# Kernel optimization log

Hardware: AMD Instinct MI355X
Metric: run time of the kernel (lower is better)

## Reference

```python
import jax, jax.numpy as jnp
import numpy as np
import math

B, S, D, H = 2, 2048, 1024, 16
DK = D // H

def setup_inputs() -> dict:
    key = jax.random.key(0)
    ks = jax.random.split(key, 12)
    sc = 1.0 / math.sqrt(D)
    q = jax.random.normal(ks[0], (B, S, D), jnp.float32)
    k = jax.random.normal(ks[1], (B, S, D), jnp.float32)
    v = jax.random.normal(ks[2], (B, S, D), jnp.float32)
    # causal mask, broadcast over batch and heads; 0 -> masked (filled with -100)
    mask = jnp.tril(jnp.ones((S, S), jnp.int32))[None, None, :, :]
    w_q = jax.random.normal(ks[3], (D, D), jnp.float32) * sc
    b_q = jnp.zeros((D,), jnp.float32)
    w_k = jax.random.normal(ks[4], (D, D), jnp.float32) * sc
    b_k = jnp.zeros((D,), jnp.float32)
    w_v = jax.random.normal(ks[5], (D, D), jnp.float32) * sc
    b_v = jnp.zeros((D,), jnp.float32)
    w_0 = jax.random.normal(ks[6], (D, D), jnp.float32) * sc
    b_0 = jnp.zeros((D,), jnp.float32)
    return {"q": q, "k": k, "v": v, "mask": mask,
            "w_q": w_q, "b_q": b_q, "w_k": w_k, "b_k": b_k,
            "w_v": w_v, "b_v": b_v, "w_0": w_0, "b_0": b_0}

def reference(q, k, v, mask, w_q, b_q, w_k, b_k, w_v, b_v, w_0, b_0):
    # projections (nn.Linear: x @ W^T + b)
    query = q @ w_q.T + b_q              # [B,S,D]
    key_ = k @ w_k.T + b_k
    value = v @ w_v.T + b_v
    # split heads -> [B,H,S,DK]
    def split(x):
        return x.reshape(B, S, H, DK).transpose(0, 2, 1, 3)
    Q, K, V = split(query), split(key_), split(value)
    scores = jnp.einsum('bhqd,bhkd->bhqk', Q, K) / math.sqrt(DK)
    scores = jnp.where(mask == 0, jnp.float32(-100.0), scores)
    attn = jax.nn.softmax(scores, axis=-1)   # dropout p=0.0 -> identity
    out = jnp.einsum('bhqk,bhkd->bhqd', attn, V)  # [B,H,S,DK]
    out = out.transpose(0, 2, 1, 3).reshape(B, S, D)
    return out @ w_0.T + b_0
```

## Files before the change

kernel.cpp:

```cpp
#include <hip/hip_runtime.h>
#include <hip/hip_bf16.h>


namespace {

typedef unsigned short u16;
typedef unsigned int u32;
typedef short bf16x8 __attribute__((ext_vector_type(8)));
typedef float f32x4 __attribute__((ext_vector_type(4)));
typedef int i32x4 __attribute__((ext_vector_type(4)));

constexpr int Bz = 2, Sq = 2048, Dm = 1024, Hh = 16, Dk = 64;
constexpr int Mr = Bz * Sq;

__device__ __forceinline__ u16 bfh(float f) {
  return __bfloat16_as_ushort(__float2bfloat16(f));
}
__device__ __forceinline__ float bfup(u16 u) {
  return __uint_as_float((u32)u << 16);
}

__device__ __forceinline__ void global_load_lds16(const u16* g, u16* lds) {
  __builtin_amdgcn_global_load_lds(
      (const __attribute__((address_space(1))) void*)g,
      (__attribute__((address_space(3))) void*)lds, 16, 0, 0);
}

struct ConvArgs {
  const float* s[7]; u16* hi[7]; u16* lo[7]; int n[7];
};

__global__ __launch_bounds__(256)
void convert_hilo(ConvArgs a) {
  const int z = blockIdx.y;
  const int n = a.n[z];
  const int i = (blockIdx.x * 256 + threadIdx.x) * 4;
  if (i >= n) return;
  const float4 v = *(const float4*)(a.s[z] + i);
  ushort4 h, l;
  h.x = bfh(v.x); l.x = bfh(v.x - bfup(h.x));
  h.y = bfh(v.y); l.y = bfh(v.y - bfup(h.y));
  h.z = bfh(v.z); l.z = bfh(v.z - bfup(h.z));
  h.w = bfh(v.w); l.w = bfh(v.w - bfup(h.w));
  *(ushort4*)(a.hi[z] + i) = h;
  *(ushort4*)(a.lo[z] + i) = l;
}

template<int OUT>
__device__ __forceinline__ void gemm_split_body(
    const u16* __restrict__ Ahi, const u16* __restrict__ Alo,
    const u16* __restrict__ Bhi, const u16* __restrict__ Blo,
    const float* __restrict__ bias, float scale,
    u16* __restrict__ Yh, u16* __restrict__ Yl, float* __restrict__ Yf)
{
  constexpr int K = 1024;
  __shared__ u16 lAh[4096], lAl[4096], lBh[4096], lBl[4096];

  const int t = threadIdx.x;
  const int w = t >> 6, l = t & 63;
  const int m0 = blockIdx.x * 128, n0 = blockIdx.y * 128;
  const int wm = (w >> 1) * 64, wn = (w & 1) * 64;
  const int kg = l >> 4, lr = l & 15;

  f32x4 acc[4][4] = {};

  for (int k0 = 0; k0 < K; k0 += 32) {
#pragma unroll
    for (int is = 0; is < 2; ++is) {
      const int s = is * 256 + w * 64 + l;
      const int row = s & 127, g = s >> 7;
      const size_t aoff = (size_t)(m0 + row) * K + k0 + g * 8;
      const size_t boff = (size_t)(n0 + row) * K + k0 + g * 8;
      const int ldso = (is * 256 + w * 64) * 8;
      global_load_lds16(Ahi + aoff, &lAh[ldso]);
      global_load_lds16(Alo + aoff, &lAl[ldso]);
      global_load_lds16(Bhi + boff, &lBh[ldso]);
      global_load_lds16(Blo + boff, &lBl[ldso]);
    }
    __syncthreads();

    bf16x8 ah[4], al[4], bh[4], bl[4];
#pragma unroll
    for (int f = 0; f < 4; ++f) {
      const int ai = kg * 1024 + (wm + f * 16 + lr) * 8;
      const int bi = kg * 1024 + (wn + f * 16 + lr) * 8;
      ah[f] = *(const bf16x8*)&lAh[ai];
      al[f] = *(const bf16x8*)&lAl[ai];
      bh[f] = *(const bf16x8*)&lBh[bi];
      bl[f] = *(const bf16x8*)&lBl[bi];
    }
#pragma unroll
    for (int mf = 0; mf < 4; ++mf)
#pragma unroll
      for (int nf = 0; nf < 4; ++nf) {
        acc[mf][nf] = __builtin_amdgcn_mfma_f32_16x16x32_bf16(ah[mf], bh[nf], acc[mf][nf], 0, 0, 0);
        acc[mf][nf] = __builtin_amdgcn_mfma_f32_16x16x32_bf16(ah[mf], bl[nf], acc[mf][nf], 0, 0, 0);
        acc[mf][nf] = __builtin_amdgcn_mfma_f32_16x16x32_bf16(al[mf], bh[nf], acc[mf][nf], 0, 0, 0);
      }
    __syncthreads();
  }

#pragma unroll
  for (int mf = 0; mf < 4; ++mf)
#pragma unroll
    for (int nf = 0; nf < 4; ++nf) {
      const int n = n0 + wn + nf * 16 + lr;
      const float bv = bias[n];
      const int mbase = m0 + wm + mf * 16 + kg * 4;
      if (OUT == 2) {
#pragma unroll
        for (int r = 0; r < 4; ++r)
          Yf[(size_t)(mbase + r) * Dm + n] = (acc[mf][nf][r] + bv) * scale;
      } else {
        u16 hi[4], lo[4];
#pragma unroll
        for (int r = 0; r < 4; ++r) {
          const float val = (acc[mf][nf][r] + bv) * scale;
          hi[r] = bfh(val);
          lo[r] = bfh(val - bfup(hi[r]));
        }
        const int bb = mbase >> 11;
        const int hh = n >> 6, dkk = n & (Dk - 1);
        if (OUT == 0) {
          const size_t base = ((size_t)(bb * Hh + hh) * Sq + (mbase & (Sq - 1))) * Dk + dkk;
#pragma unroll
          for (int r = 0; r < 4; ++r) {
            Yh[base + (size_t)r * Dk] = hi[r];
            Yl[base + (size_t)r * Dk] = lo[r];
          }
        } else {
          const size_t base = ((size_t)(bb * Hh + hh) * Dk + dkk) * Sq + (mbase & (Sq - 1));
          ushort4 H, L;
          H.x = hi[0]; H.y = hi[1]; H.z = hi[2]; H.w = hi[3];
          L.x = lo[0]; L.y = lo[1]; L.z = lo[2]; L.w = lo[3];
          *(ushort4*)(Yh + base) = H;
          *(ushort4*)(Yl + base) = L;
        }
      }
    }
}

__global__ __launch_bounds__(256, 2)
void gemm_qkv_split(const u16* xqh, const u16* xql, const u16* xkh, const u16* xkl,
                    const u16* xvh, const u16* xvl,
                    const u16* wqh, const u16* wql, const u16* wkh, const u16* wkl,
                    const u16* wvh, const u16* wvl,
                    const float* bq, const float* bk, const float* bv,
                    u16* Qhi, u16* Qlo, u16* Khi, u16* Klo, u16* Vthi, u16* Vtlo)
{
  const int z = blockIdx.z;
  if (z == 0)
    gemm_split_body<0>(xqh, xql, wqh, wql, bq, 0.125f, Qhi, Qlo, nullptr);
  else if (z == 1)
    gemm_split_body<0>(xkh, xkl, wkh, wkl, bk, 1.0f, Khi, Klo, nullptr);
  else
    gemm_split_body<1>(xvh, xvl, wvh, wvl, bv, 1.0f, Vthi, Vtlo, nullptr);
}

__global__ __launch_bounds__(256, 2)
void gemm_out_split(const u16* Ah, const u16* Al, const u16* Bh, const u16* Bl,
                    const float* bias, float* Y)
{
  gemm_split_body<2>(Ah, Al, Bh, Bl, bias, 1.0f, nullptr, nullptr, Y);
}

__global__ __launch_bounds__(256, 3)
void attn_mfma(const u16* __restrict__ Qhi, const u16* __restrict__ Qlo,
               const u16* __restrict__ Khi, const u16* __restrict__ Klo,
               const u16* __restrict__ Vthi, const u16* __restrict__ Vtlo,
               u16* __restrict__ ctxh, u16* __restrict__ ctxl)
{
  __shared__ u16 stg[2 * 8192];

  const int qt = blockIdx.x, h = blockIdx.y, b = blockIdx.z;
  const int w = threadIdx.x >> 6, l = threadIdx.x & 63;
  const int lr = l & 15, g = l >> 4;
  const int q0 = qt * 64;
  const int myq = q0 + w + 4 * lr;
  const size_t hoff  = (size_t)(b * Hh + h) * Sq * Dk;
  const size_t hofft = (size_t)(b * Hh + h) * Dk * Sq;

  bf16x8 qh[2], ql[2];
  {
    const size_t qrow = hoff + (size_t)myq * Dk;
    qh[0] = *(const bf16x8*)(Qhi + qrow + 8 * g);
    qh[1] = *(const bf16x8*)(Qhi + qrow + 32 + 8 * g);
    ql[0] = *(const bf16x8*)(Qlo + qrow + 8 * g);
    ql[1] = *(const bf16x8*)(Qlo + qrow + 32 + 8 * g);
  }

  const int NT = 2 * (qt + 1);

  auto stage = [&](int t, int bb) {
    const int k0 = t * 32;
    u16* dst = stg + bb * 8192 + (w * 256) * 8;
#pragma unroll
    for (int jj = 0; jj < 4; ++jj) {
      const int s = jj * 64 + l;
      const u16* gp;
      if (w == 0)      gp = Khi  + hoff  + (size_t)(k0 + (s & 31)) * Dk + (s >> 5) * 8;
      else if (w == 1) gp = Klo  + hoff  + (size_t)(k0 + (s & 31)) * Dk + (s >> 5) * 8;
      else if (w == 2) gp = Vthi + hofft + (size_t)(s & 63) * Sq + k0 + (s >> 6) * 8;
      else             gp = Vtlo + hofft + (size_t)(s & 63) * Sq + k0 + (s >> 6) * 8;
      global_load_lds16(gp, dst + jj * 64 * 8);
    }
  };

  f32x4 O[4] = {};
  float m = -1e30f, lsum = 0.f;

  const int hsel = g >> 1;
  const int src0 = lr + ((g & 1) << 5);
  const int src1 = src0 + 16;

  stage(0, 0);
  __syncthreads();

  for (int t = 0; t < NT; ++t) {
    const int bb = t & 1;
    const int k0 = t * 32;
    if (t + 1 < NT) stage(t + 1, bb ^ 1);

    const u16* sb = stg + bb * 8192;

    bf16x8 kh[2][2], kl[2][2];
#pragma unroll
    for (int c = 0; c < 2; ++c)
#pragma unroll
      for (int h16 = 0; h16 < 2; ++h16) {
        const int slot = (c * 4 + g) * 32 + h16 * 16 + lr;
        kh[h16][c] = *(const bf16x8*)(sb + slot * 8);
        kl[h16][c] = *(const bf16x8*)(sb + (256 + slot) * 8);
      }

    f32x4 Sv[2];
#pragma unroll
    for (int h16 = 0; h16 < 2; ++h16) {
      f32x4 sa = {}, sb2 = {};
      sa  = __builtin_amdgcn_mfma_f32_16x16x32_bf16(kh[h16][0], qh[0], sa, 0, 0, 0);
      sa  = __builtin_amdgcn_mfma_f32_16x16x32_bf16(kh[h16][0], ql[0], sa, 0, 0, 0);
      sa  = __builtin_amdgcn_mfma_f32_16x16x32_bf16(kl[h16][0], qh[0], sa, 0, 0, 0);
      sb2 = __builtin_amdgcn_mfma_f32_16x16x32_bf16(kh[h16][1], qh[1], sb2, 0, 0, 0);
      sb2 = __builtin_amdgcn_mfma_f32_16x16x32_bf16(kh[h16][1], ql[1], sb2, 0, 0, 0);
      sb2 = __builtin_amdgcn_mfma_f32_16x16x32_bf16(kl[h16][1], qh[1], sb2, 0, 0, 0);
      Sv[h16] = sa + sb2;
    }

    if (k0 + 31 >= q0) {
#pragma unroll
      for (int h16 = 0; h16 < 2; ++h16)
#pragma unroll
        for (int reg = 0; reg < 4; ++reg) {
          const int kv = k0 + h16 * 16 + 4 * g + reg;
          if (kv > myq) Sv[h16][reg] = -3.0e38f;
        }
    }

    float tmax = Sv[0][0];
#pragma unroll
    for (int r = 1; r < 4; ++r) tmax = fmaxf(tmax, Sv[0][r]);
#pragma unroll
    for (int r = 0; r < 4; ++r) tmax = fmaxf(tmax, Sv[1][r]);
    tmax = fmaxf(tmax, __shfl_xor(tmax, 16));
    tmax = fmaxf(tmax, __shfl_xor(tmax, 32));
    const float mnew = fmaxf(m, tmax);
    const float corr = __expf(m - mnew);
    m = mnew;

    float pp[2][4];
    float psum = 0.f;
#pragma unroll
    for (int h16 = 0; h16 < 2; ++h16)
#pragma unroll
      for (int r = 0; r < 4; ++r) {
        pp[h16][r] = __expf(Sv[h16][r] - m);
        psum += pp[h16][r];
      }
    psum += __shfl_xor(psum, 16);
    psum += __shfl_xor(psum, 32);
    lsum = lsum * corr + psum;
#pragma unroll
    for (int dt = 0; dt < 4; ++dt) O[dt] *= corr;

    u32 Wh[4], Wl[4];
#pragma unroll
    for (int h16 = 0; h16 < 2; ++h16)
#pragma unroll
      for (int tp = 0; tp < 2; ++tp) {
        const float p0 = pp[h16][2 * tp], p1 = pp[h16][2 * tp + 1];
        const u16 h0 = bfh(p0), h1 = bfh(p1);
        Wh[2 * h16 + tp] = (u32)h0 | ((u32)h1 << 16);
        const u16 e0 = bfh(p0 - bfup(h0)), e1 = bfh(p1 - bfup(h1));
        Wl[2 * h16 + tp] = (u32)e0 | ((u32)e1 << 16);
      }

    u32 a0 = (u32)__shfl((int)Wh[0], src0), a1 = (u32)__shfl((int)Wh[1], src0);
    u32 a2 = (u32)__shfl((int)Wh[2], src0), a3 = (u32)__shfl((int)Wh[3], src0);
    u32 b0 = (u32)__shfl((int)Wh[0], src1), b1 = (u32)__shfl((int)Wh[1], src1);
    u32 b2 = (u32)__shfl((int)Wh[2], src1), b3 = (u32)__shfl((int)Wh[3], src1);
    i32x4 th;
    th.x = (int)(hsel ? a2 : a0); th.y = (int)(hsel ? a3 : a1);
    th.z = (int)(hsel ? b2 : b0); th.w = (int)(hsel ? b3 : b1);
    const bf16x8 pbh = __builtin_bit_cast(bf16x8, th);

    a0 = (u32)__shfl((int)Wl[0], src0); a1 = (u32)__shfl((int)Wl[1], src0);
    a2 = (u32)__shfl((int)Wl[2], src0); a3 = (u32)__shfl((int)Wl[3], src0);
    b0 = (u32)__shfl((int)Wl[0], src1); b1 = (u32)__shfl((int)Wl[1], src1);
    b2 = (u32)__shfl((int)Wl[2], src1); b3 = (u32)__shfl((int)Wl[3], src1);
    i32x4 tl;
    tl.x = (int)(hsel ? a2 : a0); tl.y = (int)(hsel ? a3 : a1);
    tl.z = (int)(hsel ? b2 : b0); tl.w = (int)(hsel ? b3 : b1);
    const bf16x8 pbl = __builtin_bit_cast(bf16x8, tl);

#pragma unroll
    for (int dt = 0; dt < 4; ++dt) {
      const int vslot = 512 + g * 64 + dt * 16 + lr;
      const bf16x8 vh = *(const bf16x8*)(sb + vslot * 8);
      const bf16x8 vl = *(const bf16x8*)(sb + (vslot + 256) * 8);
      O[dt] = __builtin_amdgcn_mfma_f32_16x16x32_bf16(vh, pbh, O[dt], 0, 0, 0);
      O[dt] = __builtin_amdgcn_mfma_f32_16x16x32_bf16(vh, pbl, O[dt], 0, 0, 0);
      O[dt] = __builtin_amdgcn_mfma_f32_16x16x32_bf16(vl, pbh, O[dt], 0, 0, 0);
    }

    __syncthreads();
  }

  const float inv = 1.0f / lsum;
  const size_t base = ((size_t)(b * Sq + myq) << 10) + h * Dk + 4 * g;
#pragma unroll
  for (int dt = 0; dt < 4; ++dt) {
    u16 hi[4], lo[4];
#pragma unroll
    for (int reg = 0; reg < 4; ++reg) {
      const float o = O[dt][reg] * inv;
      hi[reg] = bfh(o);
      lo[reg] = bfh(o - bfup(hi[reg]));
    }
    ushort4 H, L;
    H.x = hi[0]; H.y = hi[1]; H.z = hi[2]; H.w = hi[3];
    L.x = lo[0]; L.y = lo[1]; L.z = lo[2]; L.w = lo[3];
    *(ushort4*)(ctxh + base + dt * 16) = H;
    *(ushort4*)(ctxl + base + dt * 16) = L;
  }
}

}

extern "C" void kernel_launch(void* const* d_in, const int* in_sizes, int n_in,
                              void* d_out, int out_size, void* d_ws, size_t ws_size,
                              hipStream_t stream)
{
  (void)in_sizes; (void)n_in; (void)out_size;

  const float* q   = (const float*)d_in[0];
  const float* k   = (const float*)d_in[1];
  const float* v   = (const float*)d_in[2];
  const float* w_q = (const float*)d_in[4];
  const float* b_q = (const float*)d_in[5];
  const float* w_k = (const float*)d_in[6];
  const float* b_k = (const float*)d_in[7];
  const float* w_v = (const float*)d_in[8];
  const float* b_v = (const float*)d_in[9];
  const float* w_0 = (const float*)d_in[10];
  const float* b_0 = (const float*)d_in[11];
  float* out = (float*)d_out;

  const size_t MB = 1024 * 1024;
  const size_t NACT = (size_t)Mr * Dm;
  const size_t NW   = (size_t)Dm * Dm;
  if (ws_size < 112 * MB) return;

  char* ws = (char*)d_ws;
  u16* xqh = (u16*)(ws + 0*MB);  u16* xql = (u16*)(ws + 8*MB);
  u16* xkh = (u16*)(ws + 16*MB); u16* xkl = (u16*)(ws + 24*MB);
  u16* xvh = (u16*)(ws + 32*MB); u16* xvl = (u16*)(ws + 40*MB);
  u16* ctxh = (u16*)(ws + 0*MB); u16* ctxl = (u16*)(ws + 8*MB);
  u16* wqh = (u16*)(ws + 48*MB); u16* wql = (u16*)(ws + 50*MB);
  u16* wkh = (u16*)(ws + 52*MB); u16* wkl = (u16*)(ws + 54*MB);
  u16* wvh = (u16*)(ws + 56*MB); u16* wvl = (u16*)(ws + 58*MB);
  u16* w0h = (u16*)(ws + 60*MB); u16* w0l = (u16*)(ws + 62*MB);
  u16* Qhi  = (u16*)(ws + 64*MB); u16* Qlo  = (u16*)(ws + 72*MB);
  u16* Khi  = (u16*)(ws + 80*MB); u16* Klo  = (u16*)(ws + 88*MB);
  u16* Vthi = (u16*)(ws + 96*MB); u16* Vtlo = (u16*)(ws + 104*MB);

  ConvArgs ca;
  ca.s[0] = q;   ca.hi[0] = xqh; ca.lo[0] = xql; ca.n[0] = (int)NACT;
  ca.s[1] = k;   ca.hi[1] = xkh; ca.lo[1] = xkl; ca.n[1] = (int)NACT;
  ca.s[2] = v;   ca.hi[2] = xvh; ca.lo[2] = xvl; ca.n[2] = (int)NACT;
  ca.s[3] = w_q; ca.hi[3] = wqh; ca.lo[3] = wql; ca.n[3] = (int)NW;
  ca.s[4] = w_k; ca.hi[4] = wkh; ca.lo[4] = wkl; ca.n[4] = (int)NW;
  ca.s[5] = w_v; ca.hi[5] = wvh; ca.lo[5] = wvl; ca.n[5] = (int)NW;
  ca.s[6] = w_0; ca.hi[6] = w0h; ca.lo[6] = w0l; ca.n[6] = (int)NW;

  convert_hilo<<<dim3(NACT / 1024, 7), 256, 0, stream>>>(ca);

  gemm_qkv_split<<<dim3(Mr / 128, Dm / 128, 3), 256, 0, stream>>>(
      xqh, xql, xkh, xkl, xvh, xvl,
      wqh, wql, wkh, wkl, wvh, wvl,
      b_q, b_k, b_v, Qhi, Qlo, Khi, Klo, Vthi, Vtlo);

  attn_mfma<<<dim3(Sq / 64, Hh, Bz), 256, 0, stream>>>(
      Qhi, Qlo, Khi, Klo, Vthi, Vtlo, ctxh, ctxl);

  gemm_out_split<<<dim3(Mr / 128, Dm / 128), 256, 0, stream>>>(
      ctxh, ctxl, w0h, w0l, b_0, out);
}
```

Measured before the change: 486.0 us.

## Stage QK GEMM epilogue via LDS, reorder attention blocks, lazy softmax rescale

The Q/K projection epilogue now stages tiles in shared memory and writes contiguous 16-element row segments instead of scattered 2-byte stores. The GEMM launch bounds rise to 3 blocks per CU. The attention grid is flattened and remapped so the longest causal query tiles launch first and are spread across XCDs. Online softmax skips rescaling unless the running max grows by more than 8, which saves exp and multiply work but lets the unnormalised exponentials grow up to e^8 before correction.

```diff
diff --git a/kernel.cpp b/kernel.cpp
--- a/kernel.cpp
+++ b/kernel.cpp
@@ -54,7 +54,11 @@
     u16* __restrict__ Yh, u16* __restrict__ Yl, float* __restrict__ Yf)
 {
   constexpr int K = 1024;
-  __shared__ u16 lAh[4096], lAl[4096], lBh[4096], lBl[4096];
+  __shared__ u16 smem[16384];
+  u16* lAh = smem;
+  u16* lAl = smem + 4096;
+  u16* lBh = smem + 8192;
+  u16* lBl = smem + 12288;
 
   const int t = threadIdx.x;
   const int w = t >> 6, l = t & 63;
@@ -100,18 +104,26 @@
     __syncthreads();
   }
 
-#pragma unroll
-  for (int mf = 0; mf < 4; ++mf)
-#pragma unroll
-    for (int nf = 0; nf < 4; ++nf) {
-      const int n = n0 + wn + nf * 16 + lr;
-      const float bv = bias[n];
-      const int mbase = m0 + wm + mf * 16 + kg * 4;
-      if (OUT == 2) {
+  if (OUT == 2) {
+#pragma unroll
+    for (int mf = 0; mf < 4; ++mf)
+#pragma unroll
+      for (int nf = 0; nf < 4; ++nf) {
+        const int n = n0 + wn + nf * 16 + lr;
+        const float bv = bias[n];
+        const int mbase = m0 + wm + mf * 16 + kg * 4;
 #pragma unroll
         for (int r = 0; r < 4; ++r)
           Yf[(size_t)(mbase + r) * Dm + n] = (acc[mf][nf][r] + bv) * scale;
-      } else {
+      }
+  } else if (OUT == 1) {
+#pragma unroll
+    for (int mf = 0; mf < 4; ++mf)
+#pragma unroll
+      for (int nf = 0; nf < 4; ++nf) {
+        const int n = n0 + wn + nf * 16 + lr;
+        const float bv = bias[n];
+        const int mbase = m0 + wm + mf * 16 + kg * 4;
         u16 hi[4], lo[4];
 #pragma unroll
         for (int r = 0; r < 4; ++r) {
@@ -121,26 +133,53 @@
         }
         const int bb = mbase >> 11;
         const int hh = n >> 6, dkk = n & (Dk - 1);
-        if (OUT == 0) {
-          const size_t base = ((size_t)(bb * Hh + hh) * Sq + (mbase & (Sq - 1))) * Dk + dkk;
-#pragma unroll
-          for (int r = 0; r < 4; ++r) {
-            Yh[base + (size_t)r * Dk] = hi[r];
-            Yl[base + (size_t)r * Dk] = lo[r];
-          }
-        } else {
-          const size_t base = ((size_t)(bb * Hh + hh) * Dk + dkk) * Sq + (mbase & (Sq - 1));
-          ushort4 H, L;
-          H.x = hi[0]; H.y = hi[1]; H.z = hi[2]; H.w = hi[3];
-          L.x = lo[0]; L.y = lo[1]; L.z = lo[2]; L.w = lo[3];
-          *(ushort4*)(Yh + base) = H;
-          *(ushort4*)(Yl + base) = L;
+        const size_t base = ((size_t)(bb * Hh + hh) * Dk + dkk) * Sq + (mbase & (Sq - 1));
+        ushort4 H, L;
+        H.x = hi[0]; H.y = hi[1]; H.z = hi[2]; H.w = hi[3];
+        L.x = lo[0]; L.y = lo[1]; L.z = lo[2]; L.w = lo[3];
+        *(ushort4*)(Yh + base) = H;
+        *(ushort4*)(Yl + base) = L;
+      }
+  } else {
+    u16* Lh = smem;
+    u16* Ll = smem + 8192;
+    const int whalf = w >> 1;
+    const int rl2 = t >> 3, seg = t & 7;
+#pragma unroll
+    for (int mf = 0; mf < 4; ++mf) {
+      __syncthreads();
+#pragma unroll
+      for (int nf = 0; nf < 4; ++nf) {
+        const int col = wn + nf * 16 + lr;
+        const float bv = bias[n0 + col];
+#pragma unroll
+        for (int r = 0; r < 4; ++r) {
+          const int rl = whalf * 16 + kg * 4 + r;
+          const float val = (acc[mf][nf][r] + bv) * scale;
+          const u16 hi = bfh(val);
+          Lh[rl * 132 + col] = hi;
+          Ll[rl * 132 + col] = bfh(val - bfup(hi));
         }
       }
-    }
-}
-
-__global__ __launch_bounds__(256, 2)
+      __syncthreads();
+      const int mm = m0 + (rl2 >> 4) * 64 + mf * 16 + (rl2 & 15);
+      const int n = n0 + seg * 16;
+      const int bb = mm >> 11, ss = mm & (Sq - 1);
+      const int hh = n >> 6, dk0 = n & (Dk - 1);
+      u16* dsth = Yh + ((size_t)(bb * Hh + hh) * Sq + ss) * Dk + dk0;
+      u16* dstl = Yl + ((size_t)(bb * Hh + hh) * Sq + ss) * Dk + dk0;
+      const u16* srch = &Lh[rl2 * 132 + seg * 16];
+      const u16* srcl = &Ll[rl2 * 132 + seg * 16];
+#pragma unroll
+      for (int j = 0; j < 4; ++j) {
+        *(ushort4*)(dsth + j * 4) = *(const ushort4*)(srch + j * 4);
+        *(ushort4*)(dstl + j * 4) = *(const ushort4*)(srcl + j * 4);
+      }
+    }
+  }
+}
+
+__global__ __launch_bounds__(256, 3)
 void gemm_qkv_split(const u16* xqh, const u16* xql, const u16* xkh, const u16* xkl,
                     const u16* xvh, const u16* xvl,
                     const u16* wqh, const u16* wql, const u16* wkh, const u16* wkl,
@@ -157,7 +196,7 @@
     gemm_split_body<1>(xvh, xvl, wvh, wvl, bv, 1.0f, Vthi, Vtlo, nullptr);
 }
 
-__global__ __launch_bounds__(256, 2)
+__global__ __launch_bounds__(256, 3)
 void gemm_out_split(const u16* Ah, const u16* Al, const u16* Bh, const u16* Bl,
                     const float* bias, float* Y)
 {
@@ -172,7 +211,12 @@
 {
   __shared__ u16 stg[2 * 8192];
 
-  const int qt = blockIdx.x, h = blockIdx.y, b = blockIdx.z;
+  const int L = blockIdx.x;
+  const int lw = (L & 7) * 128 + (L >> 3);
+  const int qt = 31 - (lw & 31);
+  const int hb = lw >> 5;
+  const int h = hb & 15, b = hb >> 4;
+
   const int w = threadIdx.x >> 6, l = threadIdx.x & 63;
   const int lr = l & 15, g = l >> 4;
   const int q0 = qt * 64;
@@ -263,9 +307,14 @@
     for (int r = 0; r < 4; ++r) tmax = fmaxf(tmax, Sv[1][r]);
     tmax = fmaxf(tmax, __shfl_xor(tmax, 16));
     tmax = fmaxf(tmax, __shfl_xor(tmax, 32));
-    const float mnew = fmaxf(m, tmax);
-    const float corr = __expf(m - mnew);
-    m = mnew;
+    if (__any(tmax > m + 8.0f)) {
+      const float mnew = fmaxf(m, tmax);
+      const float corr = __expf(m - mnew);
+      m = mnew;
+      lsum *= corr;
+#pragma unroll
+      for (int dt = 0; dt < 4; ++dt) O[dt] *= corr;
+    }
 
     float pp[2][4];
     float psum = 0.f;
@@ -278,9 +327,7 @@
       }
     psum += __shfl_xor(psum, 16);
     psum += __shfl_xor(psum, 32);
-    lsum = lsum * corr + psum;
-#pragma unroll
-    for (int dt = 0; dt < 4; ++dt) O[dt] *= corr;
+    lsum += psum;
 
     u32 Wh[4], Wl[4];
 #pragma unroll
@@ -399,7 +446,7 @@
       wqh, wql, wkh, wkl, wvh, wvl,
       b_q, b_k, b_v, Qhi, Qlo, Khi, Klo, Vthi, Vtlo);
 
-  attn_mfma<<<dim3(Sq / 64, Hh, Bz), 256, 0, stream>>>(
+  attn_mfma<<<dim3(1024), 256, 0, stream>>>(
       Qhi, Qlo, Khi, Klo, Vthi, Vtlo, ctxh, ctxl);
 
   gemm_out_split<<<dim3(Mr / 128, Dm / 128), 256, 0, stream>>>(
```

Result: no change. 482.5 us (-0.7%).
